# Kernel tuning notes

Hardware: AMD Instinct MI355X
Metric: run time of the kernel (lower is better)

Reference implementation:

```python
import jax, jax.numpy as jnp
import numpy as np

N, D, H, HD, R, K, TM = 32768, 128, 2, 64, 2, 32, 2
E_EDGES, M_MOTIFS, NG = 262144, 131072, 32
EPS = 1e-5
BETA_MAX = 5.0
GRAD_CLIP = 1.0
STATE_CLIP = 10.0
DAMPING = 1.0

def _isp(x):
    # inverse softplus of init values (params stored pre-softplus)
    return float(np.log(np.expm1(x)))

LAM2_RAW, LAM3_RAW, LAMM_RAW = _isp(1.0), _isp(0.5), _isp(1.0)
B2_RAW, B3_RAW, BM_RAW = _isp(1.0), _isp(1.0), _isp(1.0)


def layernorm(x, g, b):
    mu = x.mean(-1, keepdims=True)
    v = ((x - mu) ** 2).mean(-1, keepdims=True)
    return g * (x - mu) * jax.lax.rsqrt(v + EPS) + b


def seg_lse(s, seg, n, beta):
    # tempered logsumexp over segments: (1/beta) log sum_j exp(beta*s_j); s:[items,H] -> [n,H]
    sb = beta * s
    m = jax.ops.segment_max(sb, seg, num_segments=n)
    m = jnp.where(jnp.isfinite(m), m, 0.0)
    z = jax.ops.segment_sum(jnp.exp(sb - m[seg]), seg, num_segments=n)
    return jnp.where(z > 0, (m + jnp.log(jnp.maximum(z, 1e-30))) / beta, 0.0)


def energy(X, a_2, ln_gamma, ln_beta, W_Q2, W_K2, W_Q3, W_K3, T_tau, W_Qm, W_Km, B_mem,
           c_2, u_2, c_3, u_3, v_3, t_tau, batch):
    sp = jax.nn.softplus
    lam2, lam3, lamm = sp(LAM2_RAW), sp(LAM3_RAW), sp(LAMM_RAW)
    b2 = jnp.minimum(sp(B2_RAW), BETA_MAX)
    b3 = jnp.minimum(sp(B3_RAW), BETA_MAX)
    bm = jnp.minimum(sp(BM_RAW), BETA_MAX)
    G = layernorm(X, ln_gamma, ln_beta)
    # pairwise Q2/K2 term over edges (c_2 <- u_2) with learned per-edge bias a_2
    Q2 = jnp.einsum('nd,hzd->nhz', G, W_Q2)  # [N,H,HD]
    K2 = jnp.einsum('nd,hzd->nhz', G, W_K2)
    s2 = jnp.einsum('ehz,ehz->eh', Q2[c_2], K2[u_2]) / np.sqrt(HD) + a_2  # [E,H]
    e_pair = -lam2 * seg_lse(s2, c_2, N, b2).sum(-1)  # [N]
    # rank-R bilinear motif term over (c_3,u_3,v_3) with type embedding T_tau
    Q3 = jnp.einsum('nd,hzd->nhz', G, W_Q3).reshape(N, H, R, HD)
    K3 = jnp.einsum('nd,hzd->nhz', G, W_K3).reshape(N, H, R, HD)
    qk = jnp.einsum('mhrz,mhrz->mhr', Q3[c_3], K3[u_3])
    tv = jnp.einsum('mhrz,mhrz->mhr', T_tau[t_tau], K3[v_3])
    s3 = (qk * tv).sum(-1) / HD  # [M,H]
    e_motif = -lam3 * seg_lse(s3, c_3, N, b3).sum(-1)
    # K-slot memory term
    Qm = jnp.einsum('nd,hzd->nhz', G, W_Qm)
    Km = jnp.einsum('kd,hzd->hkz', B_mem, W_Km)
    sm = jnp.einsum('nhz,hkz->nhk', Qm, Km) / np.sqrt(HD)
    e_mem = -(lamm / bm) * jax.nn.logsumexp(bm * sm, axis=-1).sum(-1)
    e_node = 0.5 * (X * X).sum(-1) + e_pair + e_motif + e_mem
    return jax.ops.segment_sum(e_node, batch, num_segments=NG)  # per-graph energy [NG]


def setup_inputs() -> dict:
    key = jax.random.key(0)
    ks = jax.random.split(key, 16)
    inp = {}
    inp['X'] = jax.random.normal(ks[0], (N, D), jnp.float32)
    inp['c_2'] = jax.random.randint(ks[1], (E_EDGES,), 0, N)
    inp['u_2'] = jax.random.randint(ks[2], (E_EDGES,), 0, N)
    inp['c_3'] = jax.random.randint(ks[3], (M_MOTIFS,), 0, N)
    inp['u_3'] = jax.random.randint(ks[4], (M_MOTIFS,), 0, N)
    inp['v_3'] = jax.random.randint(ks[5], (M_MOTIFS,), 0, N)
    inp['t_tau'] = jax.random.randint(ks[6], (M_MOTIFS,), 0, TM)
    inp['batch'] = jnp.sort(jax.random.randint(ks[7], (N,), 0, NG))
    inp['a_2'] = 0.1 * jax.random.normal(ks[8], (E_EDGES, H), jnp.float32)
    inp['step_size'] = jnp.full((1,), 0.1, jnp.float32)
    inp['ln_gamma'] = jnp.ones((D,), jnp.float32)
    inp['ln_beta'] = jnp.zeros((D,), jnp.float32)
    s = 1.0 / np.sqrt(D)
    inp['W_Q2'] = s * jax.random.normal(ks[9], (H, HD, D), jnp.float32)
    inp['W_K2'] = s * jax.random.normal(ks[10], (H, HD, D), jnp.float32)
    inp['W_Q3'] = 0.5 * s * jax.random.normal(ks[11], (H, R * HD, D), jnp.float32)
    inp['W_K3'] = 0.5 * s * jax.random.normal(ks[12], (H, R * HD, D), jnp.float32)
    inp['T_tau'] = 0.02 * jax.random.normal(ks[13], (TM, H, R, HD), jnp.float32)
    inp['W_Qm'] = 0.5 * s * jax.random.normal(ks[14], (H, HD, D), jnp.float32)
    inp['W_Km'] = 0.5 * s * jax.random.normal(ks[15], (H, HD, D), jnp.float32)
    inp['B_mem'] = s * jax.random.normal(jax.random.fold_in(key, 99), (K, D), jnp.float32)
    return inp


def reference(X, c_2, u_2, c_3, u_3, v_3, t_tau, batch, a_2, step_size,
              ln_gamma, ln_beta, W_Q2, W_K2, W_Q3, W_K3, T_tau, W_Qm, W_Km, B_mem):
    Eg, vjp = jax.vjp(
        lambda Xv: energy(Xv, a_2, ln_gamma, ln_beta, W_Q2, W_K2, W_Q3, W_K3, T_tau,
                          W_Qm, W_Km, B_mem, c_2, u_2, c_3, u_3, v_3, t_tau, batch), X)
    gX, = vjp(jnp.ones_like(Eg))
    gnorm = jnp.linalg.norm(gX, axis=-1, keepdims=True)
    gX = gX * (GRAD_CLIP / jnp.maximum(gnorm, GRAD_CLIP))
    X_next = X - step_size[0] * DAMPING * gX
    snorm = jnp.linalg.norm(X_next, axis=-1, keepdims=True)
    X_next = X_next * (STATE_CLIP / jnp.maximum(snorm, STATE_CLIP))
    return X_next, Eg
```

## Files before the change

kernel.cpp:

```cpp
#include <hip/hip_runtime.h>
#include <hip/hip_bf16.h>
#include <math.h>

typedef __hip_bfloat16 bf16;
typedef short bf16x8 __attribute__((ext_vector_type(8)));
typedef float f32x4 __attribute__((ext_vector_type(4)));

#define N_NODES 32768
#define D_DIM 128
#define E_EDG 262144
#define M_MOT 131072
#define NG_G 32
#define F_TOT 832

__device__ __forceinline__ int pidx(int n){ return ((n & 7) << 12) | (n >> 3); }

__device__ __forceinline__ float wsum64(float v){
#pragma unroll
  for (int o = 32; o > 0; o >>= 1) v += __shfl_xor(v, o, 64);
  return v;
}
__device__ __forceinline__ float hsum32(float v){
#pragma unroll
  for (int o = 16; o > 0; o >>= 1) v += __shfl_xor(v, o, 64);
  return v;
}
__device__ __forceinline__ float hmax32(float v){
#pragma unroll
  for (int o = 16; o > 0; o >>= 1) v = fmaxf(v, __shfl_xor(v, o, 64));
  return v;
}
__device__ __forceinline__ float hsum8(float v){
#pragma unroll
  for (int o = 4; o > 0; o >>= 1) v += __shfl_xor(v, o, 64);
  return v;
}
__device__ __forceinline__ float bflo(unsigned u){ return __uint_as_float(u << 16); }
__device__ __forceinline__ float bfhi(unsigned u){ return __uint_as_float(u & 0xffff0000u); }
__device__ __forceinline__ unsigned packbf(float x, float y){
  bf16 a = __float2bfloat16(x), b = __float2bfloat16(y);
  unsigned short ua = *(unsigned short*)&a, ub = *(unsigned short*)&b;
  return (unsigned)ua | ((unsigned)ub << 16);
}
__device__ __forceinline__ void unpk8(uint4 p, float* f){
  f[0] = bflo(p.x); f[1] = bfhi(p.x); f[2] = bflo(p.y); f[3] = bfhi(p.y);
  f[4] = bflo(p.z); f[5] = bfhi(p.z); f[6] = bflo(p.w); f[7] = bfhi(p.w);
}

__global__ __launch_bounds__(256) void k_phaseA(
    const int* c2, const int* u2, const int* c3, const int* u3, const int* v3,
    const float* wq2, const float* wk2, const float* wq3, const float* wk3,
    const float* wqm, const float* wkm, const float* bmem, const float* Ttau,
    int* cnt, float* Wcat, bf16* Ttb, float* Mprod){
  __shared__ float KmL[64];
  int b = blockIdx.x, t = threadIdx.x;
  if (b < 8192){
    int range = b >> 3;
    int res = b & 7;
    int i = range * 256 + t;
    int c = c2[i], u = u2[i];
    if ((c & 7) == res) atomicAdd(&cnt[pidx(c)], 1);
    if ((u & 7) == res) atomicAdd(&cnt[N_NODES + pidx(u)], 1);
    if (i < M_MOT){
      int cc = c3[i], uu = u3[i], vv = v3[i];
      if ((cc & 7) == res) atomicAdd(&cnt[2 * N_NODES + pidx(cc)], 1);
      if ((uu & 7) == res) atomicAdd(&cnt[3 * N_NODES + pidx(uu)], 1);
      if ((vv & 7) == res) atomicAdd(&cnt[4 * N_NODES + pidx(vv)], 1);
    }
  } else if (b < 8608){
    int idx = (b - 8192) * 256 + t;
    if (idx < 768 * D_DIM){
      int f = idx / D_DIM, d = idx - f * D_DIM;
      const float* src; int fr;
      if      (f < 128){ src = wq2; fr = f; }
      else if (f < 256){ src = wk2; fr = f - 128; }
      else if (f < 512){ src = wq3; fr = f - 256; }
      else             { src = wk3; fr = f - 512; }
      Wcat[f * D_DIM + d] = src[fr * D_DIM + d];
    } else {
      int j = idx - 768 * D_DIM;
      Ttb[j] = __float2bfloat16(Ttau[j]);
    }
  } else {
    int hk = b - 8608;
    int h = hk >> 5, k = hk & 31;
    if (t < 64){
      const float* wrow = wkm + (size_t)(h * 64 + t) * D_DIM;
      const float* brow = bmem + k * D_DIM;
      float acc = 0.f;
      for (int d = 0; d < D_DIM; d++) acc += wrow[d] * brow[d];
      KmL[t] = acc;
    }
    __syncthreads();
    if (t < 128){
      const float* w = wqm + (size_t)(h * 64) * 128 + t;
      float acc = 0.f;
      for (int z = 0; z < 64; z++) acc += w[z * 128] * KmL[z];
      Mprod[t * 64 + hk] = acc;
    }
  }
}

__global__ __launch_bounds__(1024) void k_phaseB(
    int* cntcur, int* off,
    const float* X, const float* gamma, const float* beta,
    bf16* Gb, float* mu, float* rstd, float* e_node,
    const float* Wcat, const float* Mprod, bf16* wfF, bf16* wfB){
  __shared__ int sd[1024];
  int b = blockIdx.x, t = threadIdx.x;
  if (b < 5){
    int a = b;
    int* c = cntcur + a * N_NODES;
    int* o = off + a * (N_NODES + 1);
    int loc[32];
    int sum = 0;
#pragma unroll
    for (int j = 0; j < 32; j++){ loc[j] = sum; sum += c[t * 32 + j]; }
    sd[t] = sum;
    __syncthreads();
    for (int s = 1; s < 1024; s <<= 1){
      int v = (t >= s) ? sd[t - s] : 0;
      __syncthreads();
      sd[t] += v;
      __syncthreads();
    }
    int excl = sd[t] - sum;
#pragma unroll
    for (int j = 0; j < 32; j++){
      int val = excl + loc[j];
      o[t * 32 + j] = val;
      c[t * 32 + j] = val;
    }
    if (t == 1023) o[N_NODES] = sd[1023];
  } else if (b < 2053){
    int wv = t >> 6, l = t & 63;
    int n = (b - 5) * 16 + wv;
    float2 x2 = ((const float2*)(X + (size_t)n * 128))[l];
    float sumx = wsum64(x2.x + x2.y);
    float sumxx = wsum64(x2.x * x2.x + x2.y * x2.y);
    float m = sumx * (1.0f / 128.0f);
    float var = sumxx * (1.0f / 128.0f) - m * m;
    float rs = rsqrtf(var + 1e-5f);
    float2 gg = ((const float2*)gamma)[l];
    float2 bb = ((const float2*)beta)[l];
    ((unsigned*)(Gb + (size_t)n * 128))[l] =
        packbf(gg.x * (x2.x - m) * rs + bb.x, gg.y * (x2.y - m) * rs + bb.y);
    if (l == 0){ mu[n] = m; rstd[n] = rs; e_node[n] = 0.5f * sumxx; }
  } else {
    int idx = (b - 2053) * 1024 + t;
    int j = idx & 7, lane = (idx >> 3) & 63, tt = idx >> 9;
    {
      int tn = tt >> 2, kt = tt & 3;
      int f = tn * 16 + (lane & 15), d = kt * 32 + (lane >> 4) * 8 + j;
      float v = (f < 768) ? Wcat[f * 128 + d] : 0.125f * Mprod[d * 64 + (f - 768)];
      wfF[idx] = __float2bfloat16(v);
    }
    {
      int td = tt / 26, tf = tt - td * 26;
      int f = tf * 32 + (lane >> 4) * 8 + j, d = td * 16 + (lane & 15);
      float v = (f < 768) ? Wcat[f * 128 + d] : -0.125f * Mprod[d * 64 + (f - 768)];
      wfB[idx] = __float2bfloat16(v);
    }
  }
}

__global__ __launch_bounds__(256) void k_phaseC(
    const bf16* Gb, const bf16* wfF, bf16* P,
    const int* c2, const int* u2, const int* c3, const int* u3, const int* v3,
    const int* t3, int* cur,
    uint2* lec, uint2* leu, uint2* lmc, uint2* lmu, uint2* lmv){
  int b = blockIdx.x;
  int g = b / 29, r = b - g * 29;
  if (r < 13){
    __shared__ unsigned shP[64 * 36];
    int f = g * 13 + r;
    int bx = f & 511, by = f >> 9;
    int wave = threadIdx.x >> 6, lane = threadIdx.x & 63;
    int m0 = bx * 64 + wave * 16;
    int tn0 = by * 4;
    int rw = lane & 15, quad = lane >> 4;
    const bf16* aptr = Gb + (size_t)(m0 + rw) * 128 + quad * 8;
    bf16x8 a[4];
#pragma unroll
    for (int kt = 0; kt < 4; kt++) a[kt] = *(const bf16x8*)(aptr + kt * 32);
    f32x4 acc[4];
#pragma unroll
    for (int i = 0; i < 4; i++) acc[i] = (f32x4){0.f, 0.f, 0.f, 0.f};
#pragma unroll
    for (int nf = 0; nf < 4; nf++){
      int tn = tn0 + nf;
#pragma unroll
      for (int kt = 0; kt < 4; kt++){
        bf16x8 bb = *(const bf16x8*)(wfF + (((size_t)tn * 4 + kt) * 64 + lane) * 8);
        acc[nf] = __builtin_amdgcn_mfma_f32_16x16x32_bf16(bb, a[kt], acc[nf], 0, 0, 0);
      }
    }
    int lrow = wave * 16 + rw;
#pragma unroll
    for (int nf = 0; nf < 4; nf++){
      unsigned lo = packbf(acc[nf][0], acc[nf][1]);
      unsigned hi = packbf(acc[nf][2], acc[nf][3]);
      *(uint2*)&shP[lrow * 36 + nf * 8 + quad * 2] = make_uint2(lo, hi);
    }
    __syncthreads();
    int t = threadIdx.x;
    int orow = t >> 2, s = t & 3;
    uint4 v0 = *(const uint4*)&shP[orow * 36 + s * 4];
    uint4 v1 = *(const uint4*)&shP[orow * 36 + 16 + s * 4];
    uint4* prow = (uint4*)(P + (size_t)(bx * 64 + orow) * F_TOT) + tn0 * 2 + s;
    prow[0] = v0;
    prow[4] = v1;
  } else {
    int j = g * 16 + (r - 13);
    int range = j >> 3;
    int res = b & 7;
    int i = range * 256 + threadIdx.x;
    {
      int c = c2[i], u = u2[i];
      if ((c & 7) == res){
        int pos = atomicAdd(&cur[pidx(c)], 1);
        lec[pos] = make_uint2((unsigned)u, (unsigned)i);
      }
      if ((u & 7) == res){
        int pos = atomicAdd(&cur[N_NODES + pidx(u)], 1);
        leu[pos] = make_uint2((unsigned)c, (unsigned)i);
      }
    }
    if (i < M_MOT){
      int c = c3[i], u = u3[i], v = v3[i], mt = t3[i];
      if ((c & 7) == res){
        int pos = atomicAdd(&cur[2 * N_NODES + pidx(c)], 1);
        lmc[pos] = make_uint2((unsigned)(u | (v << 16)), (unsigned)(mt | (i << 5)));
      }
      if ((u & 7) == res){
        int pos = atomicAdd(&cur[3 * N_NODES + pidx(u)], 1);
        lmu[pos] = make_uint2((unsigned)c, (unsigned)i);
      }
      if ((v & 7) == res){
        int pos = atomicAdd(&cur[4 * N_NODES + pidx(v)], 1);
        lmv[pos] = make_uint2((unsigned)(c | (mt << 16)), (unsigned)i);
      }
    }
  }
}

__global__ __launch_bounds__(256) void k_fused_c(const bf16* P, const uint2* lec, const uint2* lmc,
                   const bf16* Ttb, const float* a2, const int* off_ec, const int* off_mc,
                   float* s2, float* rz2, float* s3, float* qkb, float* tvb, float* rz3,
                   bf16* dP, float* e_pair, float* e_mot, float* e_mem){
  int b = blockIdx.x;
  int type = b % 3, grp = b / 3;
  int wave = threadIdx.x >> 6, z = threadIdx.x & 63;
  int n = grp * 4 + wave;
  int l = z & 31, lh = z >> 5;
  int pn = pidx(n);

  if (type == 0){
    int q = z >> 4, l16 = z & 15, hg = l16 >> 3;
    int beg = off_ec[pn], end = off_ec[pn + 1];
    uint4 qp = ((const uint4*)(P + (size_t)n * F_TOT))[l16];
    float qv[8]; unpk8(qp, qv);
    float acc[8] = {0,0,0,0,0,0,0,0};
    float zz = 0.f;
    int iters = (end - beg + 3) >> 2;
    for (int it = 0; it < iters; it++){
      int idx = beg + 4 * it + q;
      bool valid = idx < end;
      int idc = valid ? idx : end - 1;
      uint2 pl = lec[idc];
      float2 av = *(const float2*)(a2 + (size_t)pl.y * 2);
      uint4 kp = ((const uint4*)(P + (size_t)pl.x * F_TOT + 128))[l16];
      float kv[8]; unpk8(kp, kv);
      float d = 0.f;
#pragma unroll
      for (int j = 0; j < 8; j++) d += qv[j] * kv[j];
      float s = hsum8(d) * 0.125f + (hg ? av.y : av.x);
      if (valid && (l16 & 7) == 0) s2[2 * pl.y + hg] = s;
      float ex = valid ? expf(s) : 0.f;
#pragma unroll
      for (int j = 0; j < 8; j++) acc[j] += ex * kv[j];
      zz += ex;
    }
#pragma unroll
    for (int j = 0; j < 8; j++){
      acc[j] += __shfl_xor(acc[j], 16, 64);
      acc[j] += __shfl_xor(acc[j], 32, 64);
    }
    zz += __shfl_xor(zz, 16, 64);
    zz += __shfl_xor(zz, 32, 64);
    float rz = (zz > 0.f) ? 1.0f / zz : 0.f;
    float coef = -0.125f * rz;
    if (z < 16){
      uint4 o;
      o.x = packbf(coef * acc[0], coef * acc[1]);
      o.y = packbf(coef * acc[2], coef * acc[3]);
      o.z = packbf(coef * acc[4], coef * acc[5]);
      o.w = packbf(coef * acc[6], coef * acc[7]);
      ((uint4*)(dP + (size_t)n * F_TOT))[l16] = o;
      if ((l16 & 7) == 0) rz2[n * 2 + hg] = rz;
    }
    float eterm = (zz > 0.f) ? -logf(zz) : 0.f;
    float eo = __shfl(eterm, 8, 64);
    if (z == 0) e_pair[n] = eterm + eo;
  } else if (type == 1){
    int g = l >> 3, hg = g >> 1;
    int beg = off_mc[pn], end = off_mc[pn + 1];
    uint4 qp = ((const uint4*)(P + (size_t)n * F_TOT + 256))[l];
    float qv[8]; unpk8(qp, qv);
    float acc[8] = {0,0,0,0,0,0,0,0};
    float zz = 0.f;
    int iters = (end - beg + 1) >> 1;
    for (int it = 0; it < iters; it++){
      int idx = beg + 2 * it + lh;
      bool valid = idx < end;
      int idc = valid ? idx : end - 1;
      uint2 pl = lmc[idc];
      int u = pl.x & 0xffff, v = pl.x >> 16;
      int tix = pl.y & 31; unsigned m = pl.y >> 5;
      uint4 kup = ((const uint4*)(P + (size_t)u * F_TOT + 512))[l];
      uint4 kvp = ((const uint4*)(P + (size_t)v * F_TOT + 512))[l];
      uint4 tp  = ((const uint4*)(Ttb + (size_t)tix * 256))[l];
      float k[8], vv[8], pt[8];
      unpk8(kup, k); unpk8(kvp, vv); unpk8(tp, pt);
      float dq = 0.f, dt = 0.f;
#pragma unroll
      for (int j = 0; j < 8; j++){ dq += qv[j] * k[j]; dt += pt[j] * vv[j]; }
      float qk = hsum8(dq);
      float tv = hsum8(dt);
      if (valid && (l & 7) == 0){ qkb[(size_t)4 * m + g] = qk; tvb[(size_t)4 * m + g] = tv; }
      float w = qk * tv;
      float s = (w + __shfl_xor(w, 8, 64)) * (1.0f / 64.0f);
      if (valid && (l & 15) == 0) s3[2 * m + hg] = s;
      float ex = valid ? expf(s) : 0.f;
      float et = ex * tv;
#pragma unroll
      for (int j = 0; j < 8; j++) acc[j] += et * k[j];
      zz += ex;
    }
#pragma unroll
    for (int j = 0; j < 8; j++) acc[j] += __shfl_xor(acc[j], 32, 64);
    zz += __shfl_xor(zz, 32, 64);
    float rz = (zz > 0.f) ? 1.0f / zz : 0.f;
    float coef = (-0.5f / 64.0f) * rz;
    if (z < 32){
      uint4 o;
      o.x = packbf(coef * acc[0], coef * acc[1]);
      o.y = packbf(coef * acc[2], coef * acc[3]);
      o.z = packbf(coef * acc[4], coef * acc[5]);
      o.w = packbf(coef * acc[6], coef * acc[7]);
      ((uint4*)(dP + (size_t)n * F_TOT + 256))[l] = o;
      if ((l & 15) == 0) rz3[n * 2 + hg] = rz;
    }
    float eterm = (zz > 0.f) ? -0.5f * logf(zz) : 0.f;
    float eo = __shfl(eterm, 16, 64);
    if (z == 0) e_mot[n] = eterm + eo;
  } else {
    unsigned short us = ((const unsigned short*)(P + (size_t)n * F_TOT + 768))[z];
    float s = __uint_as_float((unsigned)us << 16);
    float mx = hmax32(s);
    float ex = expf(s - mx);
    float se = hsum32(ex);
    float p = ex / se;
    bf16 pb = __float2bfloat16(p);
    ((unsigned short*)(dP + (size_t)n * F_TOT + 768))[z] = *(unsigned short*)&pb;
    float eterm = -(mx + logf(se));
    float eo = __shfl(eterm, z ^ 32, 64);
    if (z == 0) e_mem[n] = eterm + eo;
  }
}

__global__ __launch_bounds__(256) void k_phaseE(const bf16* P, const uint2* leu,
                    const uint2* lmu, const uint2* lmv, const bf16* Ttb,
                    const float* s2, const float* rz2, const float* s3, const float* rz3,
                    const float* qkb, const float* tvb,
                    const int* off_eu, const int* off_mu, const int* off_mv, bf16* dP,
                    const float* e_node, const float* e_pair, const float* e_mot,
                    const float* e_mem, const int* batch, float* Eg){
  __shared__ float eg[NG_G];
  int b = blockIdx.x;
  if (b < 128){
    int t = threadIdx.x;
    if (t < NG_G) eg[t] = 0.f;
    __syncthreads();
    int n = b * 256 + t;
    float e = e_node[n] + e_pair[n] + e_mot[n] + e_mem[n];
    atomicAdd(&eg[batch[n]], e);
    __syncthreads();
    if (t < NG_G) atomicAdd(&Eg[t], eg[t]);
    return;
  }
  int b2 = b - 128;
  int type = b2 & 1, grp = b2 >> 1;
  int wave = threadIdx.x >> 6, z = threadIdx.x & 63;
  int n = grp * 4 + wave;
  int l = z & 31, lh = z >> 5;
  int pn = pidx(n);

  if (type == 0){
    int q = z >> 4, l16 = z & 15, hg = l16 >> 3;
    int beg = off_eu[pn], end = off_eu[pn + 1];
    float acc[8] = {0,0,0,0,0,0,0,0};
    int iters = (end - beg + 3) >> 2;
    for (int it = 0; it < iters; it++){
      int idx = beg + 4 * it + q;
      bool valid = idx < end;
      int idc = valid ? idx : end - 1;
      uint2 pl = leu[idc];
      uint4 qp = ((const uint4*)(P + (size_t)pl.x * F_TOT))[l16];
      float qv[8]; unpk8(qp, qv);
      float p = valid ? expf(s2[2 * pl.y + hg]) * rz2[pl.x * 2 + hg] : 0.f;
#pragma unroll
      for (int j = 0; j < 8; j++) acc[j] += p * qv[j];
    }
#pragma unroll
    for (int j = 0; j < 8; j++){
      acc[j] += __shfl_xor(acc[j], 16, 64);
      acc[j] += __shfl_xor(acc[j], 32, 64);
    }
    if (z < 16){
      uint4 o;
      o.x = packbf(-0.125f * acc[0], -0.125f * acc[1]);
      o.y = packbf(-0.125f * acc[2], -0.125f * acc[3]);
      o.z = packbf(-0.125f * acc[4], -0.125f * acc[5]);
      o.w = packbf(-0.125f * acc[6], -0.125f * acc[7]);
      ((uint4*)(dP + (size_t)n * F_TOT + 128))[l16] = o;
    }
  } else {
    int g = l >> 3, hg = g >> 1;
    float acc[8] = {0,0,0,0,0,0,0,0};
    {
      int beg = off_mu[pn], end = off_mu[pn + 1];
      int iters = (end - beg + 1) >> 1;
      for (int it = 0; it < iters; it++){
        int idx = beg + 2 * it + lh;
        bool valid = idx < end;
        int idc = valid ? idx : end - 1;
        uint2 pl = lmu[idc];
        unsigned c = pl.x, m = pl.y;
        uint4 qp = ((const uint4*)(P + (size_t)c * F_TOT + 256))[l];
        float qv[8]; unpk8(qp, qv);
        float w = valid ? expf(s3[2 * m + hg]) * rz3[c * 2 + hg] * tvb[(size_t)4 * m + g] : 0.f;
#pragma unroll
        for (int j = 0; j < 8; j++) acc[j] += w * qv[j];
      }
    }
    {
      int beg = off_mv[pn], end = off_mv[pn + 1];
      int iters = (end - beg + 1) >> 1;
      for (int it = 0; it < iters; it++){
        int idx = beg + 2 * it + lh;
        bool valid = idx < end;
        int idc = valid ? idx : end - 1;
        uint2 pl = lmv[idc];
        unsigned c = pl.x & 0xffff, tix = pl.x >> 16, m = pl.y;
        uint4 tp = ((const uint4*)(Ttb + (size_t)tix * 256))[l];
        float pt[8]; unpk8(tp, pt);
        float w = valid ? expf(s3[2 * m + hg]) * rz3[c * 2 + hg] * qkb[(size_t)4 * m + g] : 0.f;
#pragma unroll
        for (int j = 0; j < 8; j++) acc[j] += w * pt[j];
      }
    }
#pragma unroll
    for (int j = 0; j < 8; j++) acc[j] += __shfl_xor(acc[j], 32, 64);
    const float cst = -0.5f / 64.0f;
    if (z < 32){
      uint4 o;
      o.x = packbf(cst * acc[0], cst * acc[1]);
      o.y = packbf(cst * acc[2], cst * acc[3]);
      o.z = packbf(cst * acc[4], cst * acc[5]);
      o.w = packbf(cst * acc[6], cst * acc[7]);
      ((uint4*)(dP + (size_t)n * F_TOT + 512))[l] = o;
    }
  }
}

__global__ __launch_bounds__(256) void k_bwd_mfma(const bf16* dP, const bf16* wfB, float* dG){
  int wave = threadIdx.x >> 6, lane = threadIdx.x & 63;
  int m0 = blockIdx.x * 64 + wave * 16;
  int rw = lane & 15, quad = lane >> 4;
  const bf16* aptr = dP + (size_t)(m0 + rw) * F_TOT + quad * 8;
  f32x4 acc[8];
#pragma unroll
  for (int i = 0; i < 8; i++) acc[i] = (f32x4){0.f, 0.f, 0.f, 0.f};
  for (int kt = 0; kt < 26; kt++){
    bf16x8 a = *(const bf16x8*)(aptr + kt * 32);
#pragma unroll
    for (int td = 0; td < 8; td++){
      bf16x8 b = *(const bf16x8*)(wfB + (((size_t)td * 26 + kt) * 64 + lane) * 8);
      acc[td] = __builtin_amdgcn_mfma_f32_16x16x32_bf16(a, b, acc[td], 0, 0, 0);
    }
  }
#pragma unroll
  for (int td = 0; td < 8; td++){
    int col = td * 16 + rw;
#pragma unroll
    for (int r = 0; r < 4; r++){
      int row = m0 + quad * 4 + r;
      dG[(size_t)row * 128 + col] = acc[td][r];
    }
  }
}

__global__ __launch_bounds__(256) void k_finalize(const float* X, const float* dG, const float* gamma,
                    const float* mu, const float* rstd, const float* step_p,
                    const float* Eg, float* out){
  int wave = threadIdx.x >> 6, l = threadIdx.x & 63;
  int n = blockIdx.x * 4 + wave;
  float2 x2 = ((const float2*)(X + (size_t)n * 128))[l];
  float2 dg2 = ((const float2*)(dG + (size_t)n * 128))[l];
  float2 gg = ((const float2*)gamma)[l];
  float rs = rstd[n], m = mu[n];
  float xh0 = (x2.x - m) * rs, xh1 = (x2.y - m) * rs;
  float dxh0 = dg2.x * gg.x, dxh1 = dg2.y * gg.y;
  float s1 = wsum64(dxh0 + dxh1);
  float s2v = wsum64(dxh0 * xh0 + dxh1 * xh1);
  float g0 = x2.x + rs * (dxh0 - s1 * (1.0f / 128) - xh0 * (s2v * (1.0f / 128)));
  float g1 = x2.y + rs * (dxh1 - s1 * (1.0f / 128) - xh1 * (s2v * (1.0f / 128)));
  float gn = sqrtf(wsum64(g0 * g0 + g1 * g1));
  float gc = 1.0f / fmaxf(gn, 1.0f);
  g0 *= gc; g1 *= gc;
  float step = step_p[0];
  float xn0 = x2.x - step * g0, xn1 = x2.y - step * g1;
  float sn = sqrtf(wsum64(xn0 * xn0 + xn1 * xn1));
  float sc = 10.0f / fmaxf(sn, 10.0f);
  ((float2*)(out + (size_t)n * 128))[l] = make_float2(xn0 * sc, xn1 * sc);
  if (blockIdx.x == 0 && threadIdx.x < NG_G)
    out[(size_t)N_NODES * 128 + threadIdx.x] = Eg[threadIdx.x];
}

extern "C" void kernel_launch(void* const* d_in, const int* in_sizes, int n_in,
                              void* d_out, int out_size, void* d_ws, size_t ws_size,
                              hipStream_t stream) {
  const float* X     = (const float*)d_in[0];
  const int*  c_2    = (const int*) d_in[1];
  const int*  u_2    = (const int*) d_in[2];
  const int*  c_3    = (const int*) d_in[3];
  const int*  u_3    = (const int*) d_in[4];
  const int*  v_3    = (const int*) d_in[5];
  const int*  t_tau  = (const int*) d_in[6];
  const int*  batch  = (const int*) d_in[7];
  const float* a_2   = (const float*)d_in[8];
  const float* step_s= (const float*)d_in[9];
  const float* ln_g  = (const float*)d_in[10];
  const float* ln_b  = (const float*)d_in[11];
  const float* W_Q2  = (const float*)d_in[12];
  const float* W_K2  = (const float*)d_in[13];
  const float* W_Q3  = (const float*)d_in[14];
  const float* W_K3  = (const float*)d_in[15];
  const float* T_tau = (const float*)d_in[16];
  const float* W_Qm  = (const float*)d_in[17];
  const float* W_Km  = (const float*)d_in[18];
  const float* B_mem = (const float*)d_in[19];
  float* out = (float*)d_out;

  char* wb = (char*)d_ws;
  float* Wcat   = (float*)wb; wb += 768 * D_DIM * 4;
  float* Mprod  = (float*)wb; wb += 8192 * 4;
  float* mu     = (float*)wb; wb += N_NODES * 4;
  float* rstd   = (float*)wb; wb += N_NODES * 4;
  float* s2     = (float*)wb; wb += (size_t)E_EDG * 2 * 4;
  float* rz2    = (float*)wb; wb += N_NODES * 2 * 4;
  float* s3     = (float*)wb; wb += (size_t)M_MOT * 2 * 4;
  float* qkb    = (float*)wb; wb += (size_t)M_MOT * 4 * 4;
  float* tvb    = (float*)wb; wb += (size_t)M_MOT * 4 * 4;
  float* rz3    = (float*)wb; wb += N_NODES * 2 * 4;
  float* e_node = (float*)wb; wb += N_NODES * 4;
  float* e_pair = (float*)wb; wb += N_NODES * 4;
  float* e_mot  = (float*)wb; wb += N_NODES * 4;
  float* e_mem  = (float*)wb; wb += N_NODES * 4;
  float* Eg     = (float*)wb; wb += NG_G * 4;
  float* dG     = (float*)wb; wb += (size_t)N_NODES * D_DIM * 4;
  bf16* Gb      = (bf16*)wb;  wb += (size_t)N_NODES * D_DIM * 2;
  bf16* P       = (bf16*)wb;  wb += (size_t)N_NODES * F_TOT * 2;
  bf16* dP      = (bf16*)wb;  wb += (size_t)N_NODES * F_TOT * 2;
  bf16* wfF     = (bf16*)wb;  wb += 106496 * 2;
  bf16* wfB     = (bf16*)wb;  wb += 106496 * 2;
  bf16* Ttb     = (bf16*)wb;  wb += 8192 * 2;
  int* cntcur   = (int*)wb;   wb += 5 * N_NODES * 4;
  int* off      = (int*)wb;   wb += 5 * (N_NODES + 1) * 4;
  wb = (char*)(((size_t)wb + 15) & ~(size_t)15);
  uint2* lec    = (uint2*)wb; wb += (size_t)E_EDG * 8;
  uint2* leu    = (uint2*)wb; wb += (size_t)E_EDG * 8;
  uint2* lmc    = (uint2*)wb; wb += (size_t)M_MOT * 8;
  uint2* lmu    = (uint2*)wb; wb += (size_t)M_MOT * 8;
  uint2* lmv    = (uint2*)wb; wb += (size_t)M_MOT * 8;

  const int* off_ec = off;
  const int* off_eu = off + (N_NODES + 1);
  const int* off_mc = off + 2 * (N_NODES + 1);
  const int* off_mu = off + 3 * (N_NODES + 1);
  const int* off_mv = off + 4 * (N_NODES + 1);

  hipMemsetAsync(cntcur, 0, 5 * N_NODES * sizeof(int), stream);
  hipMemsetAsync(Eg, 0, NG_G * sizeof(float), stream);
  hipLaunchKernelGGL(k_phaseA, dim3(8672), dim3(256), 0, stream,
                     c_2, u_2, c_3, u_3, v_3, W_Q2, W_K2, W_Q3, W_K3,
                     W_Qm, W_Km, B_mem, T_tau, cntcur, Wcat, Ttb, Mprod);
  hipLaunchKernelGGL(k_phaseB, dim3(2157), dim3(1024), 0, stream,
                     cntcur, off, X, ln_g, ln_b, Gb, mu, rstd, e_node,
                     Wcat, Mprod, wfF, wfB);
  hipLaunchKernelGGL(k_phaseC, dim3(512 * 29), dim3(256), 0, stream,
                     Gb, wfF, P, c_2, u_2, c_3, u_3, v_3, t_tau, cntcur,
                     lec, leu, lmc, lmu, lmv);
  hipLaunchKernelGGL(k_fused_c, dim3(3 * (N_NODES / 4)), dim3(256), 0, stream,
                     P, lec, lmc, Ttb, a_2, off_ec, off_mc,
                     s2, rz2, s3, qkb, tvb, rz3, dP, e_pair, e_mot, e_mem);
  hipLaunchKernelGGL(k_phaseE, dim3(128 + 2 * (N_NODES / 4)), dim3(256), 0, stream,
                     P, leu, lmu, lmv, Ttb, s2, rz2, s3, rz3, qkb, tvb,
                     off_eu, off_mu, off_mv, dP,
                     e_node, e_pair, e_mot, e_mem, batch, Eg);
  hipLaunchKernelGGL(k_bwd_mfma, dim3(N_NODES / 64), dim3(256), 0, stream, dP, wfB, dG);
  hipLaunchKernelGGL(k_finalize, dim3(N_NODES / 4), dim3(256), 0, stream,
                     X, dG, ln_g, mu, rstd, step_s, Eg, out);
}
```

Baseline: 381.5 us.

## Privatize degree histograms per block residue and widen per-lane gathers in backward scatter

The degree-counting stage no longer launches 8x blocks that each re-read all index arrays and keep only one residue class. Instead each block atomically increments one of 8 replicated histograms, chosen by block id, and the scan stage sums the 8 replicas before the prefix sum. This cuts redundant index reads and atomic contention, at the cost of a larger memset and a scan that reads 8x more counts. The backward gather kernel now lets each lane handle both heads with two 16-byte loads and vectorized score loads, so more edges or motifs are processed per iteration and per-edge scalar loads are amortized.

```diff
diff --git a/kernel.cpp b/kernel.cpp
--- a/kernel.cpp
+++ b/kernel.cpp
@@ -54,21 +54,18 @@
     int* cnt, float* Wcat, bf16* Ttb, float* Mprod){
   __shared__ float KmL[64];
   int b = blockIdx.x, t = threadIdx.x;
-  if (b < 8192){
-    int range = b >> 3;
-    int res = b & 7;
-    int i = range * 256 + t;
-    int c = c2[i], u = u2[i];
-    if ((c & 7) == res) atomicAdd(&cnt[pidx(c)], 1);
-    if ((u & 7) == res) atomicAdd(&cnt[N_NODES + pidx(u)], 1);
+  if (b < 1024){
+    int* base = cnt + (size_t)(b & 7) * 5 * N_NODES;
+    int i = b * 256 + t;
+    atomicAdd(&base[pidx(c2[i])], 1);
+    atomicAdd(&base[N_NODES + pidx(u2[i])], 1);
     if (i < M_MOT){
-      int cc = c3[i], uu = u3[i], vv = v3[i];
-      if ((cc & 7) == res) atomicAdd(&cnt[2 * N_NODES + pidx(cc)], 1);
-      if ((uu & 7) == res) atomicAdd(&cnt[3 * N_NODES + pidx(uu)], 1);
-      if ((vv & 7) == res) atomicAdd(&cnt[4 * N_NODES + pidx(vv)], 1);
-    }
-  } else if (b < 8608){
-    int idx = (b - 8192) * 256 + t;
+      atomicAdd(&base[2 * N_NODES + pidx(c3[i])], 1);
+      atomicAdd(&base[3 * N_NODES + pidx(u3[i])], 1);
+      atomicAdd(&base[4 * N_NODES + pidx(v3[i])], 1);
+    }
+  } else if (b < 1440){
+    int idx = (b - 1024) * 256 + t;
     if (idx < 768 * D_DIM){
       int f = idx / D_DIM, d = idx - f * D_DIM;
       const float* src; int fr;
@@ -82,7 +79,7 @@
       Ttb[j] = __float2bfloat16(Ttau[j]);
     }
   } else {
-    int hk = b - 8608;
+    int hk = b - 1440;
     int h = hk >> 5, k = hk & 31;
     if (t < 64){
       const float* wrow = wkm + (size_t)(h * 64 + t) * D_DIM;
@@ -110,12 +107,18 @@
   int b = blockIdx.x, t = threadIdx.x;
   if (b < 5){
     int a = b;
-    int* c = cntcur + a * N_NODES;
+    int* cbase = cntcur + a * N_NODES;
     int* o = off + a * (N_NODES + 1);
     int loc[32];
     int sum = 0;
 #pragma unroll
-    for (int j = 0; j < 32; j++){ loc[j] = sum; sum += c[t * 32 + j]; }
+    for (int j = 0; j < 32; j++){
+      int idx = t * 32 + j;
+      int tot = 0;
+#pragma unroll
+      for (int rr = 0; rr < 8; rr++) tot += cbase[(size_t)rr * 5 * N_NODES + idx];
+      loc[j] = sum; sum += tot;
+    }
     sd[t] = sum;
     __syncthreads();
     for (int s = 1; s < 1024; s <<= 1){
@@ -129,7 +132,7 @@
     for (int j = 0; j < 32; j++){
       int val = excl + loc[j];
       o[t * 32 + j] = val;
-      c[t * 32 + j] = val;
+      cbase[t * 32 + j] = val;
     }
     if (t == 1023) o[N_NODES] = sd[1023];
   } else if (b < 2053){
@@ -393,83 +396,135 @@
   int type = b2 & 1, grp = b2 >> 1;
   int wave = threadIdx.x >> 6, z = threadIdx.x & 63;
   int n = grp * 4 + wave;
-  int l = z & 31, lh = z >> 5;
   int pn = pidx(n);
 
   if (type == 0){
-    int q = z >> 4, l16 = z & 15, hg = l16 >> 3;
+    int e8 = z >> 3, l8 = z & 7;
     int beg = off_eu[pn], end = off_eu[pn + 1];
-    float acc[8] = {0,0,0,0,0,0,0,0};
-    int iters = (end - beg + 3) >> 2;
+    float acc[16];
+#pragma unroll
+    for (int j = 0; j < 16; j++) acc[j] = 0.f;
+    int iters = (end - beg + 7) >> 3;
     for (int it = 0; it < iters; it++){
-      int idx = beg + 4 * it + q;
+      int idx = beg + 8 * it + e8;
       bool valid = idx < end;
       int idc = valid ? idx : end - 1;
       uint2 pl = leu[idc];
-      uint4 qp = ((const uint4*)(P + (size_t)pl.x * F_TOT))[l16];
-      float qv[8]; unpk8(qp, qv);
-      float p = valid ? expf(s2[2 * pl.y + hg]) * rz2[pl.x * 2 + hg] : 0.f;
-#pragma unroll
-      for (int j = 0; j < 8; j++) acc[j] += p * qv[j];
-    }
-#pragma unroll
-    for (int j = 0; j < 8; j++){
+      const uint4* qrow = (const uint4*)(P + (size_t)pl.x * F_TOT);
+      uint4 qp0 = qrow[l8];
+      uint4 qp1 = qrow[l8 + 8];
+      float2 sv = *(const float2*)(s2 + 2 * (size_t)pl.y);
+      float2 rv = *(const float2*)(rz2 + 2 * (size_t)pl.x);
+      float qv0[8], qv1[8];
+      unpk8(qp0, qv0); unpk8(qp1, qv1);
+      float p0 = valid ? expf(sv.x) * rv.x : 0.f;
+      float p1 = valid ? expf(sv.y) * rv.y : 0.f;
+#pragma unroll
+      for (int j = 0; j < 8; j++){
+        acc[j]     += p0 * qv0[j];
+        acc[8 + j] += p1 * qv1[j];
+      }
+    }
+#pragma unroll
+    for (int j = 0; j < 16; j++){
+      acc[j] += __shfl_xor(acc[j], 8, 64);
       acc[j] += __shfl_xor(acc[j], 16, 64);
       acc[j] += __shfl_xor(acc[j], 32, 64);
     }
-    if (z < 16){
-      uint4 o;
-      o.x = packbf(-0.125f * acc[0], -0.125f * acc[1]);
-      o.y = packbf(-0.125f * acc[2], -0.125f * acc[3]);
-      o.z = packbf(-0.125f * acc[4], -0.125f * acc[5]);
-      o.w = packbf(-0.125f * acc[6], -0.125f * acc[7]);
-      ((uint4*)(dP + (size_t)n * F_TOT + 128))[l16] = o;
+    if (z < 8){
+      uint4 o0, o1;
+      o0.x = packbf(-0.125f * acc[0], -0.125f * acc[1]);
+      o0.y = packbf(-0.125f * acc[2], -0.125f * acc[3]);
+      o0.z = packbf(-0.125f * acc[4], -0.125f * acc[5]);
+      o0.w = packbf(-0.125f * acc[6], -0.125f * acc[7]);
+      o1.x = packbf(-0.125f * acc[8], -0.125f * acc[9]);
+      o1.y = packbf(-0.125f * acc[10], -0.125f * acc[11]);
+      o1.z = packbf(-0.125f * acc[12], -0.125f * acc[13]);
+      o1.w = packbf(-0.125f * acc[14], -0.125f * acc[15]);
+      uint4* dst = (uint4*)(dP + (size_t)n * F_TOT + 128);
+      dst[z] = o0;
+      dst[z + 8] = o1;
     }
   } else {
-    int g = l >> 3, hg = g >> 1;
-    float acc[8] = {0,0,0,0,0,0,0,0};
+    int m4 = z >> 4, l16 = z & 15;
+    int g0 = l16 >> 3;
+    float acc[16];
+#pragma unroll
+    for (int j = 0; j < 16; j++) acc[j] = 0.f;
     {
       int beg = off_mu[pn], end = off_mu[pn + 1];
-      int iters = (end - beg + 1) >> 1;
+      int iters = (end - beg + 3) >> 2;
       for (int it = 0; it < iters; it++){
-        int idx = beg + 2 * it + lh;
+        int idx = beg + 4 * it + m4;
         bool valid = idx < end;
         int idc = valid ? idx : end - 1;
         uint2 pl = lmu[idc];
-        unsigned c = pl.x, m = pl.y;
-        uint4 qp = ((const uint4*)(P + (size_t)c * F_TOT + 256))[l];
-        float qv[8]; unpk8(qp, qv);
-        float w = valid ? expf(s3[2 * m + hg]) * rz3[c * 2 + hg] * tvb[(size_t)4 * m + g] : 0.f;
-#pragma unroll
-        for (int j = 0; j < 8; j++) acc[j] += w * qv[j];
+        const uint4* qrow = (const uint4*)(P + (size_t)pl.x * F_TOT + 256);
+        uint4 qp0 = qrow[l16];
+        uint4 qp1 = qrow[l16 + 16];
+        float2 sv = *(const float2*)(s3 + 2 * (size_t)pl.y);
+        float2 rv = *(const float2*)(rz3 + 2 * (size_t)pl.x);
+        float4 tq = *(const float4*)(tvb + 4 * (size_t)pl.y);
+        float t0 = g0 ? tq.y : tq.x;
+        float t1 = g0 ? tq.w : tq.z;
+        float qv0[8], qv1[8];
+        unpk8(qp0, qv0); unpk8(qp1, qv1);
+        float w0 = valid ? expf(sv.x) * rv.x * t0 : 0.f;
+        float w1 = valid ? expf(sv.y) * rv.y * t1 : 0.f;
+#pragma unroll
+        for (int j = 0; j < 8; j++){
+          acc[j]     += w0 * qv0[j];
+          acc[8 + j] += w1 * qv1[j];
+        }
       }
     }
     {
       int beg = off_mv[pn], end = off_mv[pn + 1];
-      int iters = (end - beg + 1) >> 1;
+      int iters = (end - beg + 3) >> 2;
       for (int it = 0; it < iters; it++){
-        int idx = beg + 2 * it + lh;
+        int idx = beg + 4 * it + m4;
         bool valid = idx < end;
         int idc = valid ? idx : end - 1;
         uint2 pl = lmv[idc];
-        unsigned c = pl.x & 0xffff, tix = pl.x >> 16, m = pl.y;
-        uint4 tp = ((const uint4*)(Ttb + (size_t)tix * 256))[l];
-        float pt[8]; unpk8(tp, pt);
-        float w = valid ? expf(s3[2 * m + hg]) * rz3[c * 2 + hg] * qkb[(size_t)4 * m + g] : 0.f;
-#pragma unroll
-        for (int j = 0; j < 8; j++) acc[j] += w * pt[j];
-      }
-    }
-#pragma unroll
-    for (int j = 0; j < 8; j++) acc[j] += __shfl_xor(acc[j], 32, 64);
+        unsigned c = pl.x & 0xffff, tix = pl.x >> 16;
+        const uint4* trow = (const uint4*)(Ttb + (size_t)tix * 256);
+        uint4 tp0 = trow[l16];
+        uint4 tp1 = trow[l16 + 16];
+        float2 sv = *(const float2*)(s3 + 2 * (size_t)pl.y);
+        float2 rv = *(const float2*)(rz3 + 2 * (size_t)c);
+        float4 qq = *(const float4*)(qkb + 4 * (size_t)pl.y);
+        float q0 = g0 ? qq.y : qq.x;
+        float q1 = g0 ? qq.w : qq.z;
+        float pt0[8], pt1[8];
+        unpk8(tp0, pt0); unpk8(tp1, pt1);
+        float w0 = valid ? expf(sv.x) * rv.x * q0 : 0.f;
+        float w1 = valid ? expf(sv.y) * rv.y * q1 : 0.f;
+#pragma unroll
+        for (int j = 0; j < 8; j++){
+          acc[j]     += w0 * pt0[j];
+          acc[8 + j] += w1 * pt1[j];
+        }
+      }
+    }
+#pragma unroll
+    for (int j = 0; j < 16; j++){
+      acc[j] += __shfl_xor(acc[j], 16, 64);
+      acc[j] += __shfl_xor(acc[j], 32, 64);
+    }
     const float cst = -0.5f / 64.0f;
-    if (z < 32){
-      uint4 o;
-      o.x = packbf(cst * acc[0], cst * acc[1]);
-      o.y = packbf(cst * acc[2], cst * acc[3]);
-      o.z = packbf(cst * acc[4], cst * acc[5]);
-      o.w = packbf(cst * acc[6], cst * acc[7]);
-      ((uint4*)(dP + (size_t)n * F_TOT + 512))[l] = o;
+    if (z < 16){
+      uint4 o0, o1;
+      o0.x = packbf(cst * acc[0], cst * acc[1]);
+      o0.y = packbf(cst * acc[2], cst * acc[3]);
+      o0.z = packbf(cst * acc[4], cst * acc[5]);
+      o0.w = packbf(cst * acc[6], cst * acc[7]);
+      o1.x = packbf(cst * acc[8], cst * acc[9]);
+      o1.y = packbf(cst * acc[10], cst * acc[11]);
+      o1.z = packbf(cst * acc[12], cst * acc[13]);
+      o1.w = packbf(cst * acc[14], cst * acc[15]);
+      uint4* dst = (uint4*)(dP + (size_t)n * F_TOT + 512);
+      dst[l16] = o0;
+      dst[l16 + 16] = o1;
     }
   }
 }
@@ -576,7 +631,7 @@
   bf16* wfF     = (bf16*)wb;  wb += 106496 * 2;
   bf16* wfB     = (bf16*)wb;  wb += 106496 * 2;
   bf16* Ttb     = (bf16*)wb;  wb += 8192 * 2;
-  int* cntcur   = (int*)wb;   wb += 5 * N_NODES * 4;
+  int* cntcur   = (int*)wb;   wb += 8 * 5 * N_NODES * 4;
   int* off      = (int*)wb;   wb += 5 * (N_NODES + 1) * 4;
   wb = (char*)(((size_t)wb + 15) & ~(size_t)15);
   uint2* lec    = (uint2*)wb; wb += (size_t)E_EDG * 8;
@@ -591,9 +646,9 @@
   const int* off_mu = off + 3 * (N_NODES + 1);
   const int* off_mv = off + 4 * (N_NODES + 1);
 
-  hipMemsetAsync(cntcur, 0, 5 * N_NODES * sizeof(int), stream);
+  hipMemsetAsync(cntcur, 0, (size_t)8 * 5 * N_NODES * sizeof(int), stream);
   hipMemsetAsync(Eg, 0, NG_G * sizeof(float), stream);
-  hipLaunchKernelGGL(k_phaseA, dim3(8672), dim3(256), 0, stream,
+  hipLaunchKernelGGL(k_phaseA, dim3(1504), dim3(256), 0, stream,
                      c_2, u_2, c_3, u_3, v_3, W_Q2, W_K2, W_Q3, W_K3,
                      W_Qm, W_Km, B_mem, T_tau, cntcur, Wcat, Ttb, Mprod);
   hipLaunchKernelGGL(k_phaseB, dim3(2157), dim3(1024), 0, stream,
```

Measured after the change: 401.9 us. 1.05x slower.
